# Performance work log

Hardware: AMD Instinct MI355X
Metric: run time of the kernel (lower is better)

## Reference

```python
import jax, jax.numpy as jnp
import numpy as np

NUM_HEADS = 8
NUM_KV_HEADS = 1
HEAD_DIM = 256
ROPE_THETA = 10000.0


def setup_inputs() -> dict:
    key = jax.random.key(0)
    ks = jax.random.split(key, 5)
    B, S, H = 4, 2048, 2048
    hidden_states = jax.random.normal(ks[0], (B, S, H), dtype=jnp.float32)
    # Linear weights stored as (in_features, out_features); y = x @ W
    scale = 0.02
    Wq = jax.random.normal(ks[1], (H, NUM_HEADS * HEAD_DIM), dtype=jnp.float32) * scale
    Wk = jax.random.normal(ks[2], (H, NUM_KV_HEADS * HEAD_DIM), dtype=jnp.float32) * scale
    Wv = jax.random.normal(ks[3], (H, NUM_KV_HEADS * HEAD_DIM), dtype=jnp.float32) * scale
    Wo = jax.random.normal(ks[4], (NUM_HEADS * HEAD_DIM, H), dtype=jnp.float32) * scale
    position_ids = jnp.broadcast_to(jnp.arange(S, dtype=jnp.int64), (B, S))
    return {"hidden_states": hidden_states, "Wq": Wq, "Wk": Wk, "Wv": Wv,
            "Wo": Wo, "position_ids": position_ids}


def _rotate_half(x):
    h = x.shape[-1] // 2
    return jnp.concatenate([-x[..., h:], x[..., :h]], axis=-1)


def _rope_cos_sin(position_ids, head_dim, theta):
    # inv_freq: [head_dim/2]
    inv_freq = 1.0 / (theta ** (jnp.arange(0, head_dim, 2, dtype=jnp.float32) / head_dim))
    freqs = position_ids.astype(jnp.float32)[..., None] * inv_freq  # [B,S,hd/2]
    emb = jnp.concatenate([freqs, freqs], axis=-1)                   # [B,S,hd]
    # shape [B,1,S,hd] to broadcast over heads
    return jnp.cos(emb)[:, None], jnp.sin(emb)[:, None]


def reference(hidden_states, Wq, Wk, Wv, Wo, position_ids):
    B, S, H = hidden_states.shape
    groups = NUM_HEADS // NUM_KV_HEADS

    q = (hidden_states @ Wq).reshape(B, S, NUM_HEADS, HEAD_DIM).transpose(0, 2, 1, 3)
    k = (hidden_states @ Wk).reshape(B, S, NUM_KV_HEADS, HEAD_DIM).transpose(0, 2, 1, 3)
    v = (hidden_states @ Wv).reshape(B, S, NUM_KV_HEADS, HEAD_DIM).transpose(0, 2, 1, 3)

    cos, sin = _rope_cos_sin(position_ids, HEAD_DIM, ROPE_THETA)
    q = q * cos + _rotate_half(q) * sin
    k = k * cos + _rotate_half(k) * sin

    # GQA: repeat kv heads to match query heads
    k = jnp.repeat(k, groups, axis=1)  # [B,Hq,S,hd]
    v = jnp.repeat(v, groups, axis=1)

    scores = jnp.einsum('bhqd,bhkd->bhqk', q, k) / jnp.sqrt(jnp.float32(HEAD_DIM))
    causal = position_ids[:, None, :, None] >= position_ids[:, None, None, :]  # [B,1,S,S]
    scores = jnp.where(causal, scores, jnp.float32(-1e9))
    attn = jax.nn.softmax(scores, axis=-1)

    out = jnp.einsum('bhqk,bhkd->bhqd', attn, v)             # [B,H,S,hd]
    out = out.transpose(0, 2, 1, 3).reshape(B, S, NUM_HEADS * HEAD_DIM)
    return out @ Wo
```

## Files before the change

kernel.cpp:

```cpp
#include <hip/hip_runtime.h>
#include <hip/hip_bf16.h>

typedef __bf16 bf16;
typedef __bf16 bf16x8 __attribute__((ext_vector_type(8)));
typedef __bf16 bf16x4 __attribute__((ext_vector_type(4)));
typedef float f32x4 __attribute__((ext_vector_type(4)));

#define NB 4
#define SEQ 2048
#define HID 2048
#define NHEAD 8
#define HDIM 256
#define MTOT (NB*SEQ)

#define WAIT_VM8()  asm volatile("s_waitcnt vmcnt(8)" ::: "memory")
#define WAIT_VM0()  asm volatile("s_waitcnt vmcnt(0)" ::: "memory")

__device__ __forceinline__ void gl_lds16(const void* g, void* l) {
  __builtin_amdgcn_global_load_lds(
      (const __attribute__((address_space(1))) void*)g,
      (__attribute__((address_space(3))) void*)l, 16, 0, 0);
}

__global__ void cast_x_kernel(const float* __restrict__ in, bf16* __restrict__ out) {
  size_t i = (size_t)(blockIdx.x * 256 + threadIdx.x) * 8;
  float4 v0 = *(const float4*)(in + i);
  float4 v1 = *(const float4*)(in + i + 4);
  bf16x8 o;
  o[0]=(bf16)v0.x; o[1]=(bf16)v0.y; o[2]=(bf16)v0.z; o[3]=(bf16)v0.w;
  o[4]=(bf16)v1.x; o[5]=(bf16)v1.y; o[6]=(bf16)v1.z; o[7]=(bf16)v1.w;
  *(bf16x8*)(out + i) = o;
}

__global__ void transpose_cast2_kernel(const float* __restrict__ in0, bf16* __restrict__ out0,
                                       const float* __restrict__ in1, bf16* __restrict__ out1,
                                       int R, int C) {
  __shared__ float tile[32][33];
  const float* in = blockIdx.z ? in1 : in0;
  bf16* out = blockIdx.z ? out1 : out0;
  int bx = blockIdx.x * 32, by = blockIdx.y * 32;
  int tx = threadIdx.x, ty = threadIdx.y;
  #pragma unroll
  for (int k = 0; k < 4; k++)
    tile[ty + 8*k][tx] = in[(size_t)(by + ty + 8*k) * C + bx + tx];
  __syncthreads();
  #pragma unroll
  for (int k = 0; k < 4; k++)
    out[(size_t)(bx + ty + 8*k) * R + by + tx] = (bf16)tile[tx][ty + 8*k];
}

__global__ void rope_table_kernel(float2* __restrict__ tab) {
  int i = blockIdx.x * 256 + threadIdx.x;
  int s = i >> 7, p = i & 127;
  float invf = powf(10000.0f, -(float)p * (1.0f / 128.0f));
  float ang = (float)s * invf;
  float sn, cs;
  sincosf(ang, &sn, &cs);
  tab[i] = make_float2(cs, sn);
}

template<int HEADS>
__global__ void rope_apply_kernel(bf16* __restrict__ X, const float2* __restrict__ tab) {
  int i = blockIdx.x * 256 + threadIdx.x;
  int row = i / (HEADS * 32);
  int rem = i - row * (HEADS * 32);
  int h = rem >> 5;
  int p4 = (rem & 31) * 4;
  int s = row & (SEQ - 1);
  bf16* base = X + (size_t)row * (HEADS * HDIM) + h * HDIM;
  bf16x4 lo = *(bf16x4*)(base + p4);
  bf16x4 hi = *(bf16x4*)(base + p4 + 128);
  bf16x4 nlo, nhi;
  #pragma unroll
  for (int k = 0; k < 4; k++) {
    float2 cs = tab[s * 128 + p4 + k];
    float x0 = (float)lo[k], x1 = (float)hi[k];
    nlo[k] = (bf16)(x0 * cs.x - x1 * cs.y);
    nhi[k] = (bf16)(x1 * cs.x + x0 * cs.y);
  }
  *(bf16x4*)(base + p4) = nlo;
  *(bf16x4*)(base + p4 + 128) = nhi;
}

template<int EPI>
__global__ __launch_bounds__(256, 3)
void gemm_bt_kernel(const bf16* __restrict__ A, const bf16* __restrict__ Bt,
                    void* __restrict__ Cout, int N, int K,
                    bf16* __restrict__ Kout, bf16* __restrict__ VTout)
{
  __shared__ bf16 Abuf[128 * 32];
  __shared__ bf16 Bbuf[128 * 32];
  const int t = threadIdx.x;
  const int lane = t & 63, w = t >> 6;
  const int g = lane >> 4, c = lane & 15;
  const int wm = w >> 1, wn = w & 1;
  const int m0 = blockIdx.y * 128, n0 = blockIdx.x * 128;

  f32x4 acc[4][4];
  #pragma unroll
  for (int i = 0; i < 4; i++)
    #pragma unroll
    for (int j = 0; j < 4; j++)
      acc[i][j] = (f32x4){0.f, 0.f, 0.f, 0.f};

  for (int k0 = 0; k0 < K; k0 += 32) {
    #pragma unroll
    for (int it = 0; it < 2; ++it) {
      int row = it * 64 + (t >> 2);
      int part = (t & 3) ^ (row & 3);
      gl_lds16(A  + (size_t)(m0 + row) * K + k0 + part * 8, Abuf + (it * 256 + w * 64) * 8);
      gl_lds16(Bt + (size_t)(n0 + row) * K + k0 + part * 8, Bbuf + (it * 256 + w * 64) * 8);
    }
    __syncthreads();
    bf16x8 af[4], bfr[4];
    #pragma unroll
    for (int i = 0; i < 4; i++) {
      int row = wm * 64 + i * 16 + c;
      af[i] = *(const bf16x8*)((const char*)Abuf + row * 64 + ((g * 16) ^ ((c & 3) * 16)));
    }
    #pragma unroll
    for (int j = 0; j < 4; j++) {
      int row = wn * 64 + j * 16 + c;
      bfr[j] = *(const bf16x8*)((const char*)Bbuf + row * 64 + ((g * 16) ^ ((c & 3) * 16)));
    }
    #pragma unroll
    for (int i = 0; i < 4; i++)
      #pragma unroll
      for (int j = 0; j < 4; j++)
        acc[i][j] = __builtin_amdgcn_mfma_f32_16x16x32_bf16(af[i], bfr[j], acc[i][j], 0, 0, 0);
    __syncthreads();
  }

  #pragma unroll
  for (int i = 0; i < 4; i++) {
    #pragma unroll
    for (int j = 0; j < 4; j++) {
      #pragma unroll
      for (int rr = 0; rr < 4; rr++) {
        int m = m0 + wm * 64 + i * 16 + g * 4 + rr;
        int col = n0 + wn * 64 + j * 16 + c;
        float v = acc[i][j][rr];
        if constexpr (EPI == 0) {
          ((bf16*)Cout)[(size_t)m * N + col] = (bf16)v;
        } else if constexpr (EPI == 2) {
          ((float*)Cout)[(size_t)m * N + col] = v;
        } else {
          if (col < 256) {
            Kout[(size_t)m * 256 + col] = (bf16)v;
          } else {
            int b = m >> 11, s = m & 2047;
            VTout[((size_t)b * 256 + (col - 256)) * SEQ + s] = (bf16)v;
          }
        }
      }
    }
  }
}

template<int EPI>
__global__ __launch_bounds__(512, 2)
void gemm256_kernel(const bf16* __restrict__ A, const bf16* __restrict__ Bt,
                    void* __restrict__ Cout, int N, int K,
                    const float2* __restrict__ tab)
{
  __shared__ bf16 Albs[2][256 * 64];
  __shared__ bf16 Blbs[2][256 * 64];
  const int t = threadIdx.x, lane = t & 63, w = t >> 6;
  const int g = lane >> 4, c = lane & 15;
  const int wm = w >> 2, wn = w & 3;
  const int m0 = blockIdx.y * 256, n0 = blockIdx.x * 256;

  const bf16* Ab = A + (size_t)m0 * K;
  const bf16* Bb = Bt + (size_t)n0 * K;

  auto stage = [&](const bf16* G, int k0, bf16* lds) {
    #pragma unroll
    for (int it = 0; it < 4; ++it) {
      int slot = it * 512 + t;
      int row = slot >> 3, part = (slot & 7) ^ (row & 7);
      gl_lds16(G + (size_t)row * K + k0 + part * 8, lds + (it * 512 + w * 64) * 8);
    }
  };

  f32x4 acc[8][4];
  #pragma unroll
  for (int i = 0; i < 8; i++)
    #pragma unroll
    for (int j = 0; j < 4; j++)
      acc[i][j] = (f32x4){0.f, 0.f, 0.f, 0.f};

  stage(Ab, 0, &Albs[0][0]);
  stage(Bb, 0, &Blbs[0][0]);
  __builtin_amdgcn_sched_barrier(0);

  const int NT = K >> 6;
  #pragma unroll 1
  for (int kt = 0; kt < NT; ++kt) {
    const int buf = kt & 1;
    if (kt + 1 < NT) {
      stage(Ab, (kt + 1) * 64, &Albs[buf ^ 1][0]);
      stage(Bb, (kt + 1) * 64, &Blbs[buf ^ 1][0]);
    }
    __builtin_amdgcn_sched_barrier(0);
    if (kt + 1 < NT) { WAIT_VM8(); } else { WAIT_VM0(); }
    __builtin_amdgcn_s_barrier();
    __builtin_amdgcn_sched_barrier(0);

    #pragma unroll
    for (int s2 = 0; s2 < 2; s2++) {
      bf16x8 bfr[4];
      #pragma unroll
      for (int j = 0; j < 4; j++) {
        int row = (EPI == 3) ? (wn * 16 + (j & 1) * 64 + (j >> 1) * 128 + c)
                             : (wn * 64 + j * 16 + c);
        bfr[j] = *(const bf16x8*)((const char*)&Blbs[buf][0] + row * 128 +
                                  ((s2 * 64 + g * 16) ^ ((c & 7) * 16)));
      }
      #pragma unroll
      for (int i = 0; i < 8; i++) {
        int row = wm * 128 + i * 16 + c;
        const bf16x8 af = *(const bf16x8*)((const char*)&Albs[buf][0] + row * 128 +
                                           ((s2 * 64 + g * 16) ^ ((c & 7) * 16)));
        #pragma unroll
        for (int j = 0; j < 4; j++)
          acc[i][j] = __builtin_amdgcn_mfma_f32_16x16x32_bf16(af, bfr[j], acc[i][j], 0, 0, 0);
      }
    }
    __builtin_amdgcn_s_barrier();
  }

  if constexpr (EPI == 3) {
    #pragma unroll
    for (int i = 0; i < 8; i++) {
      #pragma unroll
      for (int rr = 0; rr < 4; rr++) {
        int m = m0 + wm * 128 + i * 16 + g * 4 + rr;
        int s = m & (SEQ - 1);
        bf16* orow = (bf16*)Cout + (size_t)m * N + n0;
        #pragma unroll
        for (int jp = 0; jp < 2; jp++) {
          int d = wn * 16 + jp * 64 + c;
          float2 cs = tab[s * 128 + d];
          float vlo = acc[i][jp][rr], vhi = acc[i][jp | 2][rr];
          orow[d]       = (bf16)(vlo * cs.x - vhi * cs.y);
          orow[d + 128] = (bf16)(vhi * cs.x + vlo * cs.y);
        }
      }
    }
  } else {
    #pragma unroll
    for (int i = 0; i < 8; i++) {
      #pragma unroll
      for (int j = 0; j < 4; j++) {
        #pragma unroll
        for (int rr = 0; rr < 4; rr++) {
          int m = m0 + wm * 128 + i * 16 + g * 4 + rr;
          int col = n0 + wn * 64 + j * 16 + c;
          float v = acc[i][j][rr];
          if constexpr (EPI == 0) ((bf16*)Cout)[(size_t)m * N + col] = (bf16)v;
          else                    ((float*)Cout)[(size_t)m * N + col] = v;
        }
      }
    }
  }
}

__global__ __launch_bounds__(512, 2)
void attn_kernel(const bf16* __restrict__ Q, const bf16* __restrict__ Kb,
                 const bf16* __restrict__ VT, bf16* __restrict__ O)
{
  __shared__ bf16 Klds[2][64 * 256];
  __shared__ bf16 Vlds[2][256 * 64];
  __shared__ bf16 Plds[8][16 * 64];

  const int L = blockIdx.x + ((int)gridDim.x) * blockIdx.y;
  const int xcd = L & 7, slot = L >> 3;
  const int b = xcd >> 1;
  const int rem = ((xcd & 1) << 5) | slot;
  const int h = rem >> 3;
  const int p = rem & 7;

  const int t = threadIdx.x, lane = t & 63, w = t >> 6;
  const int g = lane >> 4, c = lane & 15;

  const bf16* Kbase = Kb + (size_t)b * SEQ * HDIM;
  const bf16* Vbase = VT + (size_t)b * HDIM * SEQ;

  bf16x8 ones8;
  #pragma unroll
  for (int z = 0; z < 8; z++) ones8[z] = (bf16)1.0f;

  auto stageK = [&](int kt, int buf) {
    const int kv0 = kt * 64;
    #pragma unroll
    for (int it = 0; it < 4; ++it) {
      int slot2 = it * 512 + t;
      int krow = slot2 >> 5, kpart = (slot2 & 31) ^ (krow & 7);
      gl_lds16(Kbase + (size_t)(kv0 + krow) * HDIM + kpart * 8,
               &Klds[buf][0] + (it * 512 + w * 64) * 8);
    }
  };
  auto stageV = [&](int kt, int buf) {
    const int kv0 = kt * 64;
    #pragma unroll
    for (int it = 0; it < 4; ++it) {
      int slot2 = it * 512 + t;
      int vrow = slot2 >> 3, vpart = (slot2 & 7) ^ (vrow & 7);
      gl_lds16(Vbase + (size_t)vrow * SEQ + kv0 + vpart * 8,
               &Vlds[buf][0] + (it * 512 + w * 64) * 8);
    }
  };

  #pragma unroll 1
  for (int pass = 0; pass < 2; ++pass) {
    const int qt = pass ? (15 - p) : p;
    const int q0 = qt * 128;
    const int last = 2 * qt + 1;

    bf16x8 qf[8];
    const bf16* qp = Q + (size_t)(b * SEQ + q0 + w * 16 + c) * (NHEAD * HDIM) + h * HDIM + g * 8;
    #pragma unroll
    for (int s = 0; s < 8; s++) qf[s] = *(const bf16x8*)(qp + s * 32);
    __builtin_amdgcn_sched_barrier(0);

    stageK(0, 0);
    stageV(0, 0);
    __builtin_amdgcn_sched_barrier(0);

    f32x4 acc[16];
    #pragma unroll
    for (int f = 0; f < 16; f++) acc[f] = (f32x4){0.f, 0.f, 0.f, 0.f};
    f32x4 acc_s = (f32x4){0.f, 0.f, 0.f, 0.f};

    #pragma unroll 1
    for (int kt = 0; kt <= last; ++kt) {
      const int kv0 = kt * 64;
      const int buf = kt & 1;

      if (kt < last) { stageK(kt + 1, buf ^ 1); stageV(kt + 1, buf ^ 1); }
      __builtin_amdgcn_sched_barrier(0);
      if (kt < last) { WAIT_VM8(); } else { WAIT_VM0(); }
      __builtin_amdgcn_s_barrier();
      __builtin_amdgcn_sched_barrier(0);

      const int qrow_min = q0 + w * 16;
      if (kv0 <= qrow_min + 15) {
        f32x4 sc[4];
        #pragma unroll
        for (int j = 0; j < 4; j++) sc[j] = (f32x4){0.f, 0.f, 0.f, 0.f};
        __builtin_amdgcn_s_setprio(1);
        #pragma unroll
        for (int s = 0; s < 8; s++) {
          #pragma unroll
          for (int j = 0; j < 4; j++) {
            const bf16x8 kf = *(const bf16x8*)((const char*)&Klds[buf][0] + (j * 16 + c) * 512 +
                                               ((s * 64 + g * 16) ^ ((c & 7) * 16)));
            sc[j] = __builtin_amdgcn_mfma_f32_16x16x32_bf16(qf[s], kf, sc[j], 0, 0, 0);
          }
        }
        __builtin_amdgcn_s_setprio(0);

        const float C1 = 0.09016844f;
        const float C2 = 11.54156036f;
        const bool diag = (kv0 + 63 > qrow_min);
        #pragma unroll
        for (int rr = 0; rr < 4; rr++) {
          const int row = g * 4 + rr;
          const int qrow = qrow_min + row;
          #pragma unroll
          for (int j = 0; j < 4; j++) {
            float e = exp2f(__builtin_fmaf(sc[j][rr], C1, -C2));
            if (diag && (kv0 + j * 16 + c > qrow)) e = 0.f;
            *(bf16*)((char*)&Plds[w][0] + row * 128 + (((j * 32) + c * 2) ^ ((row & 7) << 4))) = (bf16)e;
          }
        }

        #pragma unroll
        for (int s2 = 0; s2 < 2; s2++) {
          const bf16x8 pf = *(const bf16x8*)((const char*)&Plds[w][0] + c * 128 +
                                             (((s2 * 4 + g) << 4) ^ ((c & 7) << 4)));
          __builtin_amdgcn_s_setprio(1);
          #pragma unroll
          for (int f = 0; f < 16; f++) {
            const bf16x8 vf = *(const bf16x8*)((const char*)&Vlds[buf][0] + (f * 16 + c) * 128 +
                                               ((s2 * 64 + g * 16) ^ ((c & 7) * 16)));
            acc[f] = __builtin_amdgcn_mfma_f32_16x16x32_bf16(pf, vf, acc[f], 0, 0, 0);
          }
          acc_s = __builtin_amdgcn_mfma_f32_16x16x32_bf16(pf, ones8, acc_s, 0, 0, 0);
          __builtin_amdgcn_s_setprio(0);
        }
      }

      __builtin_amdgcn_s_barrier();
    }

    #pragma unroll
    for (int rr = 0; rr < 4; rr++) {
      float inv = 1.0f / acc_s[rr];
      #pragma unroll
      for (int f = 0; f < 16; f++) {
        float v = acc[f][rr] * inv;
        O[(size_t)(b * SEQ + q0 + w * 16 + g * 4 + rr) * (NHEAD * HDIM) + h * HDIM + f * 16 + c] = (bf16)v;
      }
    }
  }
}

extern "C" void kernel_launch(void* const* d_in, const int* in_sizes, int n_in,
                              void* d_out, int out_size, void* d_ws, size_t ws_size,
                              hipStream_t stream) {
  const float* hs = (const float*)d_in[0];
  const float* Wq = (const float*)d_in[1];
  const float* Wk = (const float*)d_in[2];
  const float* Wv = (const float*)d_in[3];
  const float* Wo = (const float*)d_in[4];

  char* ws = (char*)d_ws;
  bf16* Xb   = (bf16*)(ws + 0);
  bf16* WqT  = (bf16*)(ws + 33554432);
  bf16* WkT  = (bf16*)(ws + 41943040);
  bf16* WvT  = (bf16*)(ws + 42991616);
  bf16* WoT  = (bf16*)(ws + 44040192);
  bf16* Qb   = (bf16*)(ws + 52428800);
  bf16* Kb   = (bf16*)(ws + 85983232);
  bf16* VTb  = (bf16*)(ws + 90177536);
  float2* tab = (float2*)(ws + 94371840);

  cast_x_kernel<<<8192, 256, 0, stream>>>(hs, Xb);
  transpose_cast2_kernel<<<dim3(64, 64, 2), dim3(32, 8), 0, stream>>>(Wq, WqT, Wo, WoT, 2048, 2048);
  transpose_cast2_kernel<<<dim3(8, 64, 2),  dim3(32, 8), 0, stream>>>(Wk, WkT, Wv, WvT, 2048, 256);
  rope_table_kernel<<<1024, 256, 0, stream>>>(tab);

  gemm256_kernel<3><<<dim3(8, 32), 512, 0, stream>>>(Xb, WqT, (void*)Qb, 2048, 2048, tab);
  gemm_bt_kernel<1><<<dim3(4, 64), 256, 0, stream>>>(Xb, WkT, nullptr, 512, 2048, Kb, VTb);

  rope_apply_kernel<1><<<1024, 256, 0, stream>>>(Kb, tab);

  attn_kernel<<<dim3(8, 32), 512, 0, stream>>>(Qb, Kb, VTb, Xb );

  gemm256_kernel<2><<<dim3(8, 32), 512, 0, stream>>>(Xb, WoT, d_out, 2048, 2048, nullptr);
}
```

Measured before the change: 330.7 us.

## Single-buffer attention LDS and split passes into separate blocks for occupancy

The attention kernel drops the double-buffered K/V LDS tiles and instead loads each tile synchronously, waiting on all outstanding loads before computing. The two causal passes per block are split into separate blocks, doubling the grid and raising the launch-bounds occupancy hint from 2 to 4 blocks per CU. The aim is to hide memory latency through more resident waves rather than in-block prefetch, at the cost of losing load/compute overlap within a block and adding register pressure under the tighter bound.

```diff
diff --git a/kernel.cpp b/kernel.cpp
--- a/kernel.cpp
+++ b/kernel.cpp
@@ -265,20 +265,24 @@
   }
 }
 
-__global__ __launch_bounds__(512, 2)
+__global__ __launch_bounds__(512, 4)
 void attn_kernel(const bf16* __restrict__ Q, const bf16* __restrict__ Kb,
                  const bf16* __restrict__ VT, bf16* __restrict__ O)
 {
-  __shared__ bf16 Klds[2][64 * 256];
-  __shared__ bf16 Vlds[2][256 * 64];
+  __shared__ bf16 Klds[64 * 256];
+  __shared__ bf16 Vlds[256 * 64];
   __shared__ bf16 Plds[8][16 * 64];
 
   const int L = blockIdx.x + ((int)gridDim.x) * blockIdx.y;
   const int xcd = L & 7, slot = L >> 3;
   const int b = xcd >> 1;
-  const int rem = ((xcd & 1) << 5) | slot;
-  const int h = rem >> 3;
-  const int p = rem & 7;
+  const int x = xcd & 1;
+  const int hi = slot >> 5, u = slot & 31;
+  const int h = (x << 2) | (u >> 3);
+  const int qpos = u & 7;
+  const int qt = hi ? (15 - qpos) : qpos;
+  const int q0 = qt * 128;
+  const int last = 2 * qt + 1;
 
   const int t = threadIdx.x, lane = t & 63, w = t >> 6;
   const int g = lane >> 4, c = lane & 15;
@@ -290,118 +294,107 @@
   #pragma unroll
   for (int z = 0; z < 8; z++) ones8[z] = (bf16)1.0f;
 
-  auto stageK = [&](int kt, int buf) {
+  auto stageK = [&](int kt) {
     const int kv0 = kt * 64;
     #pragma unroll
     for (int it = 0; it < 4; ++it) {
       int slot2 = it * 512 + t;
       int krow = slot2 >> 5, kpart = (slot2 & 31) ^ (krow & 7);
       gl_lds16(Kbase + (size_t)(kv0 + krow) * HDIM + kpart * 8,
-               &Klds[buf][0] + (it * 512 + w * 64) * 8);
+               Klds + (it * 512 + w * 64) * 8);
     }
   };
-  auto stageV = [&](int kt, int buf) {
+  auto stageV = [&](int kt) {
     const int kv0 = kt * 64;
     #pragma unroll
     for (int it = 0; it < 4; ++it) {
       int slot2 = it * 512 + t;
       int vrow = slot2 >> 3, vpart = (slot2 & 7) ^ (vrow & 7);
       gl_lds16(Vbase + (size_t)vrow * SEQ + kv0 + vpart * 8,
-               &Vlds[buf][0] + (it * 512 + w * 64) * 8);
+               Vlds + (it * 512 + w * 64) * 8);
     }
   };
 
+  bf16x8 qf[8];
+  const bf16* qp = Q + (size_t)(b * SEQ + q0 + w * 16 + c) * (NHEAD * HDIM) + h * HDIM + g * 8;
+  #pragma unroll
+  for (int s = 0; s < 8; s++) qf[s] = *(const bf16x8*)(qp + s * 32);
+  __builtin_amdgcn_sched_barrier(0);
+
+  f32x4 acc[16];
+  #pragma unroll
+  for (int f = 0; f < 16; f++) acc[f] = (f32x4){0.f, 0.f, 0.f, 0.f};
+  f32x4 acc_s = (f32x4){0.f, 0.f, 0.f, 0.f};
+
   #pragma unroll 1
-  for (int pass = 0; pass < 2; ++pass) {
-    const int qt = pass ? (15 - p) : p;
-    const int q0 = qt * 128;
-    const int last = 2 * qt + 1;
-
-    bf16x8 qf[8];
-    const bf16* qp = Q + (size_t)(b * SEQ + q0 + w * 16 + c) * (NHEAD * HDIM) + h * HDIM + g * 8;
-    #pragma unroll
-    for (int s = 0; s < 8; s++) qf[s] = *(const bf16x8*)(qp + s * 32);
+  for (int kt = 0; kt <= last; ++kt) {
+    const int kv0 = kt * 64;
+
+    stageK(kt);
+    stageV(kt);
     __builtin_amdgcn_sched_barrier(0);
-
-    stageK(0, 0);
-    stageV(0, 0);
+    WAIT_VM0();
+    __builtin_amdgcn_s_barrier();
     __builtin_amdgcn_sched_barrier(0);
 
-    f32x4 acc[16];
-    #pragma unroll
-    for (int f = 0; f < 16; f++) acc[f] = (f32x4){0.f, 0.f, 0.f, 0.f};
-    f32x4 acc_s = (f32x4){0.f, 0.f, 0.f, 0.f};
-
-    #pragma unroll 1
-    for (int kt = 0; kt <= last; ++kt) {
-      const int kv0 = kt * 64;
-      const int buf = kt & 1;
-
-      if (kt < last) { stageK(kt + 1, buf ^ 1); stageV(kt + 1, buf ^ 1); }
-      __builtin_amdgcn_sched_barrier(0);
-      if (kt < last) { WAIT_VM8(); } else { WAIT_VM0(); }
-      __builtin_amdgcn_s_barrier();
-      __builtin_amdgcn_sched_barrier(0);
-
-      const int qrow_min = q0 + w * 16;
-      if (kv0 <= qrow_min + 15) {
-        f32x4 sc[4];
-        #pragma unroll
-        for (int j = 0; j < 4; j++) sc[j] = (f32x4){0.f, 0.f, 0.f, 0.f};
+    const int qrow_min = q0 + w * 16;
+    if (kv0 <= qrow_min + 15) {
+      f32x4 sc[4];
+      #pragma unroll
+      for (int j = 0; j < 4; j++) sc[j] = (f32x4){0.f, 0.f, 0.f, 0.f};
+      __builtin_amdgcn_s_setprio(1);
+      #pragma unroll
+      for (int s = 0; s < 8; s++) {
+        #pragma unroll
+        for (int j = 0; j < 4; j++) {
+          const bf16x8 kf = *(const bf16x8*)((const char*)Klds + (j * 16 + c) * 512 +
+                                             ((s * 64 + g * 16) ^ ((c & 7) * 16)));
+          sc[j] = __builtin_amdgcn_mfma_f32_16x16x32_bf16(qf[s], kf, sc[j], 0, 0, 0);
+        }
+      }
+      __builtin_amdgcn_s_setprio(0);
+
+      const float C1 = 0.09016844f;
+      const float C2 = 11.54156036f;
+      const bool diag = (kv0 + 63 > qrow_min);
+      #pragma unroll
+      for (int rr = 0; rr < 4; rr++) {
+        const int row = g * 4 + rr;
+        const int qrow = qrow_min + row;
+        #pragma unroll
+        for (int j = 0; j < 4; j++) {
+          float e = exp2f(__builtin_fmaf(sc[j][rr], C1, -C2));
+          if (diag && (kv0 + j * 16 + c > qrow)) e = 0.f;
+          *(bf16*)((char*)&Plds[w][0] + row * 128 + (((j * 32) + c * 2) ^ ((row & 7) << 4))) = (bf16)e;
+        }
+      }
+
+      #pragma unroll
+      for (int s2 = 0; s2 < 2; s2++) {
+        const bf16x8 pf = *(const bf16x8*)((const char*)&Plds[w][0] + c * 128 +
+                                           (((s2 * 4 + g) << 4) ^ ((c & 7) << 4)));
         __builtin_amdgcn_s_setprio(1);
         #pragma unroll
-        for (int s = 0; s < 8; s++) {
-          #pragma unroll
-          for (int j = 0; j < 4; j++) {
-            const bf16x8 kf = *(const bf16x8*)((const char*)&Klds[buf][0] + (j * 16 + c) * 512 +
-                                               ((s * 64 + g * 16) ^ ((c & 7) * 16)));
-            sc[j] = __builtin_amdgcn_mfma_f32_16x16x32_bf16(qf[s], kf, sc[j], 0, 0, 0);
-          }
-        }
+        for (int f = 0; f < 16; f++) {
+          const bf16x8 vf = *(const bf16x8*)((const char*)Vlds + (f * 16 + c) * 128 +
+                                             ((s2 * 64 + g * 16) ^ ((c & 7) * 16)));
+          acc[f] = __builtin_amdgcn_mfma_f32_16x16x32_bf16(pf, vf, acc[f], 0, 0, 0);
+        }
+        acc_s = __builtin_amdgcn_mfma_f32_16x16x32_bf16(pf, ones8, acc_s, 0, 0, 0);
         __builtin_amdgcn_s_setprio(0);
-
-        const float C1 = 0.09016844f;
-        const float C2 = 11.54156036f;
-        const bool diag = (kv0 + 63 > qrow_min);
-        #pragma unroll
-        for (int rr = 0; rr < 4; rr++) {
-          const int row = g * 4 + rr;
-          const int qrow = qrow_min + row;
-          #pragma unroll
-          for (int j = 0; j < 4; j++) {
-            float e = exp2f(__builtin_fmaf(sc[j][rr], C1, -C2));
-            if (diag && (kv0 + j * 16 + c > qrow)) e = 0.f;
-            *(bf16*)((char*)&Plds[w][0] + row * 128 + (((j * 32) + c * 2) ^ ((row & 7) << 4))) = (bf16)e;
-          }
-        }
-
-        #pragma unroll
-        for (int s2 = 0; s2 < 2; s2++) {
-          const bf16x8 pf = *(const bf16x8*)((const char*)&Plds[w][0] + c * 128 +
-                                             (((s2 * 4 + g) << 4) ^ ((c & 7) << 4)));
-          __builtin_amdgcn_s_setprio(1);
-          #pragma unroll
-          for (int f = 0; f < 16; f++) {
-            const bf16x8 vf = *(const bf16x8*)((const char*)&Vlds[buf][0] + (f * 16 + c) * 128 +
-                                               ((s2 * 64 + g * 16) ^ ((c & 7) * 16)));
-            acc[f] = __builtin_amdgcn_mfma_f32_16x16x32_bf16(pf, vf, acc[f], 0, 0, 0);
-          }
-          acc_s = __builtin_amdgcn_mfma_f32_16x16x32_bf16(pf, ones8, acc_s, 0, 0, 0);
-          __builtin_amdgcn_s_setprio(0);
-        }
-      }
-
-      __builtin_amdgcn_s_barrier();
-    }
-
-    #pragma unroll
-    for (int rr = 0; rr < 4; rr++) {
-      float inv = 1.0f / acc_s[rr];
-      #pragma unroll
-      for (int f = 0; f < 16; f++) {
-        float v = acc[f][rr] * inv;
-        O[(size_t)(b * SEQ + q0 + w * 16 + g * 4 + rr) * (NHEAD * HDIM) + h * HDIM + f * 16 + c] = (bf16)v;
-      }
+      }
+    }
+
+    __builtin_amdgcn_s_barrier();
+  }
+
+  #pragma unroll
+  for (int rr = 0; rr < 4; rr++) {
+    float inv = 1.0f / acc_s[rr];
+    #pragma unroll
+    for (int f = 0; f < 16; f++) {
+      float v = acc[f][rr] * inv;
+      O[(size_t)(b * SEQ + q0 + w * 16 + g * 4 + rr) * (NHEAD * HDIM) + h * HDIM + f * 16 + c] = (bf16)v;
     }
   }
 }
@@ -436,7 +429,7 @@
 
   rope_apply_kernel<1><<<1024, 256, 0, stream>>>(Kb, tab);
 
-  attn_kernel<<<dim3(8, 32), 512, 0, stream>>>(Qb, Kb, VTb, Xb );
+  attn_kernel<<<dim3(8, 64), 512, 0, stream>>>(Qb, Kb, VTb, Xb );
 
   gemm256_kernel<2><<<dim3(8, 32), 512, 0, stream>>>(Xb, WoT, d_out, 2048, 2048, nullptr);
 }
```

Measured after the change: 528.0 us. 59.7% more time.

## Rework attention kernel onto 32x32 MFMA with register-resident P

Applied to the files above, without the earlier changes.

Rewrites the attention kernel to use 32x32x16 bf16 MFMAs, computing transposed score tiles with K as the A operand. The probabilities now stay in registers: they are packed with v_cvt_pk_bf16 and rearranged with v_permlane32_swap, replacing the LDS round trip through Plds. Row sums are accumulated directly in registers instead of through an extra MFMA against a ones vector. Each block now handles one 256-row query tile in a single pass instead of two balanced 128-row passes, which adds causal load imbalance across blocks and raises register pressure.

```diff
diff --git a/kernel.cpp b/kernel.cpp
--- a/kernel.cpp
+++ b/kernel.cpp
@@ -5,6 +5,7 @@
 typedef __bf16 bf16x8 __attribute__((ext_vector_type(8)));
 typedef __bf16 bf16x4 __attribute__((ext_vector_type(4)));
 typedef float f32x4 __attribute__((ext_vector_type(4)));
+typedef float f32x16 __attribute__((ext_vector_type(16)));
 
 #define NB 4
 #define SEQ 2048
@@ -20,6 +21,15 @@
   __builtin_amdgcn_global_load_lds(
       (const __attribute__((address_space(1))) void*)g,
       (__attribute__((address_space(3))) void*)l, 16, 0, 0);
+}
+
+__device__ __forceinline__ unsigned cvtpk_bf16(float lo, float hi) {
+  unsigned r;
+  asm("v_cvt_pk_bf16_f32 %0, %1, %2" : "=v"(r) : "v"(lo), "v"(hi));
+  return r;
+}
+__device__ __forceinline__ void permswap32(unsigned& a, unsigned& b) {
+  asm volatile("v_permlane32_swap_b32 %0, %1" : "+v"(a), "+v"(b));
 }
 
 __global__ void cast_x_kernel(const float* __restrict__ in, bf16* __restrict__ out) {
@@ -271,31 +281,28 @@
 {
   __shared__ bf16 Klds[2][64 * 256];
   __shared__ bf16 Vlds[2][256 * 64];
-  __shared__ bf16 Plds[8][16 * 64];
-
-  const int L = blockIdx.x + ((int)gridDim.x) * blockIdx.y;
+
+  const int L = blockIdx.x + 8 * blockIdx.y;
   const int xcd = L & 7, slot = L >> 3;
   const int b = xcd >> 1;
-  const int rem = ((xcd & 1) << 5) | slot;
-  const int h = rem >> 3;
-  const int p = rem & 7;
+  const int h = ((xcd & 1) << 2) | (slot & 3);
+  const int ti = slot >> 2;
+  const int last = 4 * ti + 3;
 
   const int t = threadIdx.x, lane = t & 63, w = t >> 6;
-  const int g = lane >> 4, c = lane & 15;
+  const int lq = lane & 31, hi = lane >> 5;
+  const int q0w = ti * 256 + w * 32;
+  const int q = q0w + lq;
 
   const bf16* Kbase = Kb + (size_t)b * SEQ * HDIM;
   const bf16* Vbase = VT + (size_t)b * HDIM * SEQ;
 
-  bf16x8 ones8;
-  #pragma unroll
-  for (int z = 0; z < 8; z++) ones8[z] = (bf16)1.0f;
-
   auto stageK = [&](int kt, int buf) {
     const int kv0 = kt * 64;
     #pragma unroll
     for (int it = 0; it < 4; ++it) {
       int slot2 = it * 512 + t;
-      int krow = slot2 >> 5, kpart = (slot2 & 31) ^ (krow & 7);
+      int krow = slot2 >> 5, kpart = (slot2 & 31) ^ (krow & 31);
       gl_lds16(Kbase + (size_t)(kv0 + krow) * HDIM + kpart * 8,
                &Klds[buf][0] + (it * 512 + w * 64) * 8);
     }
@@ -311,97 +318,106 @@
     }
   };
 
+  stageK(0, 0);
+  stageV(0, 0);
+  __builtin_amdgcn_sched_barrier(0);
+
+  bf16x8 qf[16];
+  {
+    const bf16* qp = Q + (size_t)(b * SEQ + q) * (NHEAD * HDIM) + h * HDIM + hi * 8;
+    #pragma unroll
+    for (int ch = 0; ch < 16; ch++) qf[ch] = *(const bf16x8*)(qp + ch * 16);
+  }
+  __builtin_amdgcn_sched_barrier(0);
+
+  f32x16 acc[8];
+  #pragma unroll
+  for (int dt = 0; dt < 8; dt++)
+    #pragma unroll
+    for (int r = 0; r < 16; r++) acc[dt][r] = 0.f;
+  float acc_s = 0.f;
+
+  const float C1 = 0.09016844f;
+  const float C2 = 11.54156036f;
+
   #pragma unroll 1
-  for (int pass = 0; pass < 2; ++pass) {
-    const int qt = pass ? (15 - p) : p;
-    const int q0 = qt * 128;
-    const int last = 2 * qt + 1;
-
-    bf16x8 qf[8];
-    const bf16* qp = Q + (size_t)(b * SEQ + q0 + w * 16 + c) * (NHEAD * HDIM) + h * HDIM + g * 8;
-    #pragma unroll
-    for (int s = 0; s < 8; s++) qf[s] = *(const bf16x8*)(qp + s * 32);
+  for (int kt = 0; kt <= last; ++kt) {
+    const int kv0 = kt * 64;
+    const int buf = kt & 1;
+
+    if (kt < last) { stageK(kt + 1, buf ^ 1); stageV(kt + 1, buf ^ 1); }
     __builtin_amdgcn_sched_barrier(0);
-
-    stageK(0, 0);
-    stageV(0, 0);
+    if (kt < last) { WAIT_VM8(); } else { WAIT_VM0(); }
+    __builtin_amdgcn_s_barrier();
     __builtin_amdgcn_sched_barrier(0);
 
-    f32x4 acc[16];
-    #pragma unroll
-    for (int f = 0; f < 16; f++) acc[f] = (f32x4){0.f, 0.f, 0.f, 0.f};
-    f32x4 acc_s = (f32x4){0.f, 0.f, 0.f, 0.f};
-
-    #pragma unroll 1
-    for (int kt = 0; kt <= last; ++kt) {
-      const int kv0 = kt * 64;
-      const int buf = kt & 1;
-
-      if (kt < last) { stageK(kt + 1, buf ^ 1); stageV(kt + 1, buf ^ 1); }
-      __builtin_amdgcn_sched_barrier(0);
-      if (kt < last) { WAIT_VM8(); } else { WAIT_VM0(); }
-      __builtin_amdgcn_s_barrier();
-      __builtin_amdgcn_sched_barrier(0);
-
-      const int qrow_min = q0 + w * 16;
-      if (kv0 <= qrow_min + 15) {
-        f32x4 sc[4];
-        #pragma unroll
-        for (int j = 0; j < 4; j++) sc[j] = (f32x4){0.f, 0.f, 0.f, 0.f};
+    if (kv0 <= q0w + 31) {
+      const int thr = q0w + lq - kv0;
+      #pragma unroll
+      for (int sub = 0; sub < 2; sub++) {
+        f32x16 sc;
+        #pragma unroll
+        for (int r = 0; r < 16; r++) sc[r] = 0.f;
         __builtin_amdgcn_s_setprio(1);
         #pragma unroll
-        for (int s = 0; s < 8; s++) {
-          #pragma unroll
-          for (int j = 0; j < 4; j++) {
-            const bf16x8 kf = *(const bf16x8*)((const char*)&Klds[buf][0] + (j * 16 + c) * 512 +
-                                               ((s * 64 + g * 16) ^ ((c & 7) * 16)));
-            sc[j] = __builtin_amdgcn_mfma_f32_16x16x32_bf16(qf[s], kf, sc[j], 0, 0, 0);
-          }
+        for (int ch = 0; ch < 16; ch++) {
+          const int row = sub * 32 + lq;
+          const bf16x8 kf = *(const bf16x8*)((const char*)&Klds[buf][0] + row * 512 +
+                                             (((ch * 2 + hi) ^ lq) * 16));
+          sc = __builtin_amdgcn_mfma_f32_32x32x16_bf16(kf, qf[ch], sc, 0, 0, 0);
         }
         __builtin_amdgcn_s_setprio(0);
 
-        const float C1 = 0.09016844f;
-        const float C2 = 11.54156036f;
-        const bool diag = (kv0 + 63 > qrow_min);
-        #pragma unroll
-        for (int rr = 0; rr < 4; rr++) {
-          const int row = g * 4 + rr;
-          const int qrow = qrow_min + row;
-          #pragma unroll
-          for (int j = 0; j < 4; j++) {
-            float e = exp2f(__builtin_fmaf(sc[j][rr], C1, -C2));
-            if (diag && (kv0 + j * 16 + c > qrow)) e = 0.f;
-            *(bf16*)((char*)&Plds[w][0] + row * 128 + (((j * 32) + c * 2) ^ ((row & 7) << 4))) = (bf16)e;
-          }
-        }
-
-        #pragma unroll
-        for (int s2 = 0; s2 < 2; s2++) {
-          const bf16x8 pf = *(const bf16x8*)((const char*)&Plds[w][0] + c * 128 +
-                                             (((s2 * 4 + g) << 4) ^ ((c & 7) << 4)));
+        float e[16];
+        #pragma unroll
+        for (int r = 0; r < 16; r++) {
+          float ev = exp2f(__builtin_fmaf(sc[r], C1, -C2));
+          const int kvl = sub * 32 + (r & 3) + 8 * (r >> 2) + 4 * hi;
+          ev = (kvl > thr) ? 0.f : ev;
+          e[r] = ev;
+          acc_s += ev;
+        }
+
+        #pragma unroll
+        for (int kc2 = 0; kc2 < 2; kc2++) {
+          unsigned wA = cvtpk_bf16(e[8 * kc2 + 0], e[8 * kc2 + 1]);
+          unsigned wB = cvtpk_bf16(e[8 * kc2 + 2], e[8 * kc2 + 3]);
+          unsigned wC = cvtpk_bf16(e[8 * kc2 + 4], e[8 * kc2 + 5]);
+          unsigned wD = cvtpk_bf16(e[8 * kc2 + 6], e[8 * kc2 + 7]);
+          permswap32(wA, wC);
+          permswap32(wB, wD);
+          union { unsigned u[4]; bf16x8 v; } pw;
+          pw.u[0] = wA; pw.u[1] = wB; pw.u[2] = wC; pw.u[3] = wD;
+
+          const int kc = sub * 2 + kc2;
           __builtin_amdgcn_s_setprio(1);
           #pragma unroll
-          for (int f = 0; f < 16; f++) {
-            const bf16x8 vf = *(const bf16x8*)((const char*)&Vlds[buf][0] + (f * 16 + c) * 128 +
-                                               ((s2 * 64 + g * 16) ^ ((c & 7) * 16)));
-            acc[f] = __builtin_amdgcn_mfma_f32_16x16x32_bf16(pf, vf, acc[f], 0, 0, 0);
+          for (int dt = 0; dt < 8; dt++) {
+            const int drow = dt * 32 + lq;
+            const bf16x8 vf = *(const bf16x8*)((const char*)&Vlds[buf][0] + drow * 128 +
+                                               (((kc * 2 + hi) ^ (drow & 7)) * 16));
+            acc[dt] = __builtin_amdgcn_mfma_f32_32x32x16_bf16(vf, pw.v, acc[dt], 0, 0, 0);
           }
-          acc_s = __builtin_amdgcn_mfma_f32_16x16x32_bf16(pf, ones8, acc_s, 0, 0, 0);
           __builtin_amdgcn_s_setprio(0);
         }
       }
-
-      __builtin_amdgcn_s_barrier();
-    }
-
-    #pragma unroll
-    for (int rr = 0; rr < 4; rr++) {
-      float inv = 1.0f / acc_s[rr];
-      #pragma unroll
-      for (int f = 0; f < 16; f++) {
-        float v = acc[f][rr] * inv;
-        O[(size_t)(b * SEQ + q0 + w * 16 + g * 4 + rr) * (NHEAD * HDIM) + h * HDIM + f * 16 + c] = (bf16)v;
-      }
+    }
+
+    __builtin_amdgcn_s_barrier();
+  }
+
+  float s2 = __shfl(acc_s, lane ^ 32, 64);
+  float inv = 1.0f / (acc_s + s2);
+  bf16* orow = O + (size_t)(b * SEQ + q) * (NHEAD * HDIM) + h * HDIM;
+  #pragma unroll
+  for (int dt = 0; dt < 8; dt++) {
+    #pragma unroll
+    for (int g2 = 0; g2 < 4; g2++) {
+      const int d = dt * 32 + g2 * 8 + 4 * hi;
+      bf16x4 o4;
+      #pragma unroll
+      for (int rr = 0; rr < 4; rr++) o4[rr] = (bf16)(acc[dt][g2 * 4 + rr] * inv);
+      *(bf16x4*)(orow + d) = o4;
     }
   }
 }
```

Result: slower. 421.4 us (+27.4%).
